# Performance work log

Hardware: AMD Instinct MI355X
Metric: run time of the kernel (lower is better)

Reference implementation:

```python
import jax, jax.numpy as jnp
import numpy as np
import math

# Equal-size graphs make SAGPooling's top-k static; removed edges are kept with a validity mask.
B, N0, D, H, HID, POS, DEG = 64, 400, 128, 4, 64, 16, 16
C = D // H                     # per-head dim = 32
EG = N0 * DEG                  # edges per graph
E = B * EG                     # 409600 edges total
RATIO = 0.8
K1 = math.ceil(RATIO * N0)     # 320
K2 = math.ceil(RATIO * K1)     # 256
K3 = math.ceil(RATIO * K2)     # 205
KS = (K1, K2, K3)
EPS = 1e-5

def _lin(x, W, b):
    return x @ W + b

def _ln(x, g, b):
    mu = x.mean(-1, keepdims=True)
    var = ((x - mu) ** 2).mean(-1, keepdims=True)
    return (x - mu) * jax.lax.rsqrt(var + EPS) * g + b

def _bn(x, g, b):  # BatchNorm1d, training mode (biased batch variance)
    mu = x.mean(0)
    var = ((x - mu) ** 2).mean(0)
    return (x - mu) * jax.lax.rsqrt(var + EPS) * g + b

def _transformer_conv(x, src, dst, mask, Wq, bq, Wk, bk, Wv, bv, Ws, bs, N):
    # PyG TransformerConv (concat=True, root_weight=True): scatter-softmax attention over edges
    q = _lin(x, Wq, bq).reshape(N, H, C)
    k = _lin(x, Wk, bk).reshape(N, H, C)
    v = _lin(x, Wv, bv).reshape(N, H, C)
    logits = jnp.einsum('ehc,ehc->eh', q[dst], k[src]) / jnp.sqrt(jnp.float32(C))
    logits = jnp.where(mask[:, None], logits, -1e9)
    m = jnp.maximum(jax.ops.segment_max(logits, dst, num_segments=N), -1e9)
    w = jnp.exp(logits - m[dst]) * mask[:, None]
    denom = jax.ops.segment_sum(w, dst, num_segments=N)
    alpha = w / jnp.where(denom[dst] > 0, denom[dst], 1.0)  # [E,H]
    msg = jax.ops.segment_sum(v[src] * alpha[:, :, None], dst, num_segments=N)
    return msg.reshape(N, D) + _lin(x, Ws, bs)

def _gt_block(x, src, dst, mask, Wq, bq, Wk, bk, Wv, bv, Ws, bs,
              Wlo, blo, g1, be1, W1, b1, W2, b2, g2, be2, N):
    out1 = _lin(_transformer_conv(x, src, dst, mask, Wq, bq, Wk, bk, Wv, bv, Ws, bs, N), Wlo, blo)
    out2 = _ln(out1 + x, g1, be1)
    out3 = _lin(jax.nn.relu(_lin(out2, W1, b1)), W2, b2)
    return _ln(out3 + out2, g2, be2)

def _sag_pool(x, src, dst, mask, Wrel, brel, Wroot, n, k):
    # SAGPooling: GraphConv(aggr='add') scorer, tanh nonlinearity, per-graph top-k, filter_adj via mask
    Nn = B * n
    agg = jax.ops.segment_sum(x[src] * mask[:, None], dst, num_segments=Nn)
    s = jnp.tanh((agg @ Wrel + brel + x @ Wroot)[:, 0])
    tv, ti = jax.lax.top_k(s.reshape(B, n), k)  # [B,k]
    perm = (ti + jnp.arange(B, dtype=ti.dtype)[:, None] * n).reshape(-1)
    x_new = x[perm] * tv.reshape(-1, 1)
    kept = jnp.zeros(Nn, bool).at[perm].set(True)
    new_id = jnp.zeros(Nn, jnp.int32).at[perm].set(jnp.arange(B * k, dtype=jnp.int32))
    nm = mask & kept[src] & kept[dst]
    return x_new, jnp.where(nm, new_id[src], 0), jnp.where(nm, new_id[dst], 0), nm

def _forward(x, lap_pos_enc, W_pos, b_pos,
             gt_Wq, gt_bq, gt_Wk, gt_bk, gt_Wv, gt_bv, gt_Wskip, gt_bskip,
             gt_Wlo, gt_blo, gt_ln1g, gt_ln1b, gt_W1, gt_b1, gt_W2, gt_b2, gt_ln2g, gt_ln2b,
             pool_Wrel, pool_brel, pool_Wroot,
             hW1, hb1, hW2, hb2, hW3, hb3, bn1g, bn1b, bn2g, bn2b,
             edge_src, edge_dst):
    x = x + _lin(lap_pos_enc, W_pos, b_pos)
    src, dst = edge_src, edge_dst
    mask = jnp.ones(src.shape, bool)
    n = N0
    feats = []
    for i in range(3):
        x = _gt_block(x, src, dst, mask,
                      gt_Wq[i], gt_bq[i], gt_Wk[i], gt_bk[i], gt_Wv[i], gt_bv[i],
                      gt_Wskip[i], gt_bskip[i], gt_Wlo[i], gt_blo[i],
                      gt_ln1g[i], gt_ln1b[i], gt_W1[i], gt_b1[i], gt_W2[i], gt_b2[i],
                      gt_ln2g[i], gt_ln2b[i], B * n)
        x, src, dst, mask = _sag_pool(x, src, dst, mask, pool_Wrel[i], pool_brel[i], pool_Wroot[i], n, KS[i])
        n = KS[i]
        xg = x.reshape(B, n, D)
        feats.append(jnp.concatenate([xg.max(1), xg.mean(1)], axis=1))  # [B, 2D] = gmp | gap
    xf = feats[0] + feats[1] + feats[2]
    h = jax.nn.relu(_bn(_lin(xf, hW1, hb1), bn1g, bn1b))
    h = jax.nn.relu(_bn(_lin(h, hW2, hb2), bn2g, bn2b))
    return _lin(h, hW3, hb3)[:, 0]  # [B]

def setup_inputs():
    key = jax.random.key(0)
    ks = jax.random.split(key, 16)
    rn = lambda k, shape, fan: jax.random.normal(k, shape, jnp.float32) / np.float32(np.sqrt(fan))
    inp = {}
    inp['x'] = jax.random.normal(ks[0], (B * N0, D), jnp.float32)
    inp['lap_pos_enc'] = jax.random.normal(ks[1], (B * N0, POS), jnp.float32)
    offs = (jnp.arange(B, dtype=jnp.int32) * N0)[:, None]
    inp['edge_src'] = (jax.random.randint(ks[2], (B, EG), 0, N0, jnp.int32) + offs).reshape(-1)
    inp['edge_dst'] = (jax.random.randint(ks[3], (B, EG), 0, N0, jnp.int32) + offs).reshape(-1)
    inp['W_pos'] = rn(ks[4], (POS, D), POS); inp['b_pos'] = jnp.zeros(D)
    pk = jax.random.split(ks[5], 12)
    inp['gt_Wq'] = rn(pk[0], (3, D, D), D); inp['gt_bq'] = jnp.zeros((3, D))
    inp['gt_Wk'] = rn(pk[1], (3, D, D), D); inp['gt_bk'] = jnp.zeros((3, D))
    inp['gt_Wv'] = rn(pk[2], (3, D, D), D); inp['gt_bv'] = jnp.zeros((3, D))
    inp['gt_Wskip'] = rn(pk[3], (3, D, D), D); inp['gt_bskip'] = jnp.zeros((3, D))
    inp['gt_Wlo'] = rn(pk[4], (3, D, D), D); inp['gt_blo'] = jnp.zeros((3, D))
    inp['gt_ln1g'] = jnp.ones((3, D)); inp['gt_ln1b'] = jnp.zeros((3, D))
    inp['gt_W1'] = rn(pk[5], (3, D, HID), D); inp['gt_b1'] = jnp.zeros((3, HID))
    inp['gt_W2'] = rn(pk[6], (3, HID, D), HID); inp['gt_b2'] = jnp.zeros((3, D))
    inp['gt_ln2g'] = jnp.ones((3, D)); inp['gt_ln2b'] = jnp.zeros((3, D))
    inp['pool_Wrel'] = rn(pk[7], (3, D, 1), D); inp['pool_brel'] = jnp.zeros((3, 1))
    inp['pool_Wroot'] = rn(pk[8], (3, D, 1), D)
    inp['hW1'] = rn(pk[9], (2 * D, D), 2 * D); inp['hb1'] = jnp.zeros(D)
    inp['hW2'] = rn(pk[10], (D, D // 2), D); inp['hb2'] = jnp.zeros(D // 2)
    inp['hW3'] = rn(pk[11], (D // 2, 1), D // 2); inp['hb3'] = jnp.zeros(1)
    inp['bn1g'] = jnp.ones(D); inp['bn1b'] = jnp.zeros(D)
    inp['bn2g'] = jnp.ones(D // 2); inp['bn2b'] = jnp.zeros(D // 2)
    return inp

def reference(x, lap_pos_enc, edge_src, edge_dst, W_pos, b_pos,
              gt_Wq, gt_bq, gt_Wk, gt_bk, gt_Wv, gt_bv, gt_Wskip, gt_bskip,
              gt_Wlo, gt_blo, gt_ln1g, gt_ln1b, gt_W1, gt_b1, gt_W2, gt_b2, gt_ln2g, gt_ln2b,
              pool_Wrel, pool_brel, pool_Wroot,
              hW1, hb1, hW2, hb2, hW3, hb3, bn1g, bn1b, bn2g, bn2b):
    return _forward(x, lap_pos_enc, W_pos, b_pos,
                    gt_Wq, gt_bq, gt_Wk, gt_bk, gt_Wv, gt_bv, gt_Wskip, gt_bskip,
                    gt_Wlo, gt_blo, gt_ln1g, gt_ln1b, gt_W1, gt_b1, gt_W2, gt_b2, gt_ln2g, gt_ln2b,
                    pool_Wrel, pool_brel, pool_Wroot,
                    hW1, hb1, hW2, hb2, hW3, hb3, bn1g, bn1b, bn2g, bn2b,
                    edge_src, edge_dst)
```

## Files before the change

kernel.cpp:

```cpp
#include <hip/hip_runtime.h>
#include <math.h>

#define BB   64
#define NPG0 400
#define DD   128
#define HH   4
#define CC   32
#define HIDD 64
#define POSD 16
#define EE   409600
#define EG   6400

__global__ void k_pos(const float* __restrict__ x, const float* __restrict__ lap,
                      const float* __restrict__ Wp, const float* __restrict__ bp,
                      float* __restrict__ out, int N){
  __shared__ float W[POSD*DD];
  __shared__ float bsh[DD];
  for(int i=threadIdx.x;i<POSD*DD;i+=blockDim.x) W[i]=Wp[i];
  for(int i=threadIdx.x;i<DD;i+=blockDim.x) bsh[i]=bp[i];
  __syncthreads();
  int total=N*DD;
  for(int idx=blockIdx.x*blockDim.x+threadIdx.x; idx<total; idx+=gridDim.x*blockDim.x){
    int n=idx>>7, d=idx&127;
    const float* lr=lap+(size_t)n*POSD;
    float acc=bsh[d]+x[idx];
    #pragma unroll
    for(int p=0;p<POSD;p++) acc=fmaf(lr[p],W[p*DD+d],acc);
    out[idx]=acc;
  }
}

template<int DIN,int DOUT,int EPI>
__global__ __launch_bounds__(512) void k_gemm_rt(
    const float* __restrict__ X, const float* __restrict__ Wg,
    const float* __restrict__ bias, const float* __restrict__ resid,
    const float* __restrict__ gam, const float* __restrict__ bet,
    float* __restrict__ Y){
  constexpr int BM=64;
  constexpr int CG=DOUT/4;
  constexpr int RS=512/CG;
  constexpr int RPT=BM/RS;
  constexpr int XPAD=DIN+4;
  __shared__ float Wl[DIN*DOUT];
  __shared__ float Xl[BM*XPAD];
  int tid=threadIdx.x;
  { const float4* ws=(const float4*)Wg; float4* wd=(float4*)Wl;
    for(int i=tid;i<DIN*DOUT/4;i+=512) wd[i]=ws[i]; }
  { const float4* xs=(const float4*)(X+(size_t)blockIdx.x*BM*DIN);
    for(int i=tid;i<BM*DIN/4;i+=512){
      int r=i/(DIN/4), kq=i%(DIN/4);
      *(float4*)&Xl[r*XPAD+kq*4]=xs[i];
    } }
  __syncthreads();
  int cg=tid%CG, rs=tid/CG;
  float acc[RPT][4];
  #pragma unroll
  for(int j=0;j<RPT;j++){acc[j][0]=0.f;acc[j][1]=0.f;acc[j][2]=0.f;acc[j][3]=0.f;}
  for(int kt=0;kt<DIN/4;kt++){
    float4 w0=*(const float4*)&Wl[(4*kt+0)*DOUT+cg*4];
    float4 w1=*(const float4*)&Wl[(4*kt+1)*DOUT+cg*4];
    float4 w2=*(const float4*)&Wl[(4*kt+2)*DOUT+cg*4];
    float4 w3=*(const float4*)&Wl[(4*kt+3)*DOUT+cg*4];
    #pragma unroll
    for(int j=0;j<RPT;j++){
      float4 xv=*(const float4*)&Xl[(rs+RS*j)*XPAD+4*kt];
      acc[j][0]=fmaf(xv.x,w0.x,fmaf(xv.y,w1.x,fmaf(xv.z,w2.x,fmaf(xv.w,w3.x,acc[j][0]))));
      acc[j][1]=fmaf(xv.x,w0.y,fmaf(xv.y,w1.y,fmaf(xv.z,w2.y,fmaf(xv.w,w3.y,acc[j][1]))));
      acc[j][2]=fmaf(xv.x,w0.z,fmaf(xv.y,w1.z,fmaf(xv.z,w2.z,fmaf(xv.w,w3.z,acc[j][2]))));
      acc[j][3]=fmaf(xv.x,w0.w,fmaf(xv.y,w1.w,fmaf(xv.z,w2.w,fmaf(xv.w,w3.w,acc[j][3]))));
    }
  }
  float4 bv=((const float4*)bias)[cg];
  #pragma unroll
  for(int j=0;j<RPT;j++){
    int row=blockIdx.x*BM + rs+RS*j;
    float4 v;
    v.x=acc[j][0]+bv.x; v.y=acc[j][1]+bv.y; v.z=acc[j][2]+bv.z; v.w=acc[j][3]+bv.w;
    if(EPI==1){
      v.x=fmaxf(v.x,0.f); v.y=fmaxf(v.y,0.f); v.z=fmaxf(v.z,0.f); v.w=fmaxf(v.w,0.f);
    }
    if(EPI==2){
      float4 rv=*(const float4*)&resid[(size_t)row*DOUT+cg*4];
      v.x+=rv.x; v.y+=rv.y; v.z+=rv.z; v.w+=rv.w;
      float ssum=v.x+v.y+v.z+v.w;
      #pragma unroll
      for(int off=CG/2;off;off>>=1) ssum+=__shfl_xor(ssum,off);
      float mu=ssum*(1.f/DOUT);
      float dx=v.x-mu, dy=v.y-mu, dz=v.z-mu, dw=v.w-mu;
      float vsum=dx*dx+dy*dy+dz*dz+dw*dw;
      #pragma unroll
      for(int off=CG/2;off;off>>=1) vsum+=__shfl_xor(vsum,off);
      float inv=1.0f/sqrtf(vsum*(1.f/DOUT)+1e-5f);
      float4 g4=((const float4*)gam)[cg];
      float4 b4=((const float4*)bet)[cg];
      v.x=dx*inv*g4.x+b4.x; v.y=dy*inv*g4.y+b4.y;
      v.z=dz*inv*g4.z+b4.z; v.w=dw*inv*g4.w+b4.w;
    }
    *(float4*)&Y[(size_t)row*DOUT+cg*4]=v;
  }
}

__global__ __launch_bounds__(512) void k_gemm4(
    const float* __restrict__ X,
    const float* __restrict__ W0c,const float* __restrict__ W1c,
    const float* __restrict__ W2c,const float* __restrict__ W3c,
    const float* __restrict__ b0c,const float* __restrict__ b1c,
    const float* __restrict__ b2c,const float* __restrict__ b3c,
    float* __restrict__ Y0c,float* __restrict__ Y1c,
    float* __restrict__ Y2c,float* __restrict__ Y3c){
  constexpr int BM=64, CG=32, RS=16, RPT=4, XPAD=132;
  __shared__ float Wl[DD*DD];
  __shared__ float Xl[BM*XPAD];
  int tid=threadIdx.x;
  { const float4* xs=(const float4*)(X+(size_t)blockIdx.x*BM*DD);
    for(int i=tid;i<BM*32;i+=512){
      int r=i>>5, kq=i&31;
      *(float4*)&Xl[r*XPAD+kq*4]=xs[i];
    } }
  int cg=tid%CG, rs=tid/CG;
  auto one=[&](const float* __restrict__ Wg,const float* __restrict__ bias,float* __restrict__ Y){
    __syncthreads();
    { const float4* ws=(const float4*)Wg; float4* wd=(float4*)Wl;
      for(int i=tid;i<DD*32;i+=512) wd[i]=ws[i]; }
    __syncthreads();
    float acc[RPT][4];
    #pragma unroll
    for(int j=0;j<RPT;j++){acc[j][0]=0.f;acc[j][1]=0.f;acc[j][2]=0.f;acc[j][3]=0.f;}
    for(int kt=0;kt<32;kt++){
      float4 w0=*(const float4*)&Wl[(4*kt+0)*DD+cg*4];
      float4 w1=*(const float4*)&Wl[(4*kt+1)*DD+cg*4];
      float4 w2=*(const float4*)&Wl[(4*kt+2)*DD+cg*4];
      float4 w3=*(const float4*)&Wl[(4*kt+3)*DD+cg*4];
      #pragma unroll
      for(int j=0;j<RPT;j++){
        float4 xv=*(const float4*)&Xl[(rs+RS*j)*XPAD+4*kt];
        acc[j][0]=fmaf(xv.x,w0.x,fmaf(xv.y,w1.x,fmaf(xv.z,w2.x,fmaf(xv.w,w3.x,acc[j][0]))));
        acc[j][1]=fmaf(xv.x,w0.y,fmaf(xv.y,w1.y,fmaf(xv.z,w2.y,fmaf(xv.w,w3.y,acc[j][1]))));
        acc[j][2]=fmaf(xv.x,w0.z,fmaf(xv.y,w1.z,fmaf(xv.z,w2.z,fmaf(xv.w,w3.z,acc[j][2]))));
        acc[j][3]=fmaf(xv.x,w0.w,fmaf(xv.y,w1.w,fmaf(xv.z,w2.w,fmaf(xv.w,w3.w,acc[j][3]))));
      }
    }
    float4 bv=((const float4*)bias)[cg];
    #pragma unroll
    for(int j=0;j<RPT;j++){
      int row=blockIdx.x*BM + rs+RS*j;
      float4 v;
      v.x=acc[j][0]+bv.x; v.y=acc[j][1]+bv.y; v.z=acc[j][2]+bv.z; v.w=acc[j][3]+bv.w;
      *(float4*)&Y[(size_t)row*DD+cg*4]=v;
    }
  };
  one(W0c,b0c,Y0c);
  one(W1c,b1c,Y1c);
  one(W2c,b2c,Y2c);
  one(W3c,b3c,Y3c);
}

__global__ __launch_bounds__(512) void k_csr(const int* __restrict__ src,const int* __restrict__ dst,
   const int* __restrict__ msk,const int* __restrict__ kept,const int* __restrict__ nid,int n,
   int* __restrict__ rowstart,int* __restrict__ rowcnt,int* __restrict__ esrc,
   int* __restrict__ nsrc,int* __restrict__ ndst,int* __restrict__ nmsk){
  __shared__ int cnt[512];
  __shared__ int woff[512];
  int b=blockIdx.x, t=threadIdx.x;
  cnt[t]=0;
  __syncthreads();
  int ebase=b*EG, nbase=b*n;
  for(int j=t;j<EG;j+=512){
    int e=ebase+j;
    int s,d,m;
    if(kept){
      int s0=src[e], d0=dst[e];
      m=(msk?msk[e]:1) && kept[s0] && kept[d0];
      s=m?nid[s0]:0; d=m?nid[d0]:0;
      nsrc[e]=s; ndst[e]=d; nmsk[e]=m;
    } else { s=src[e]; d=dst[e]; m=1; }
    if(m) atomicAdd(&cnt[d-nbase],1);
  }
  __syncthreads();
  int v=cnt[t];
  woff[t]=v;
  __syncthreads();
  for(int off=1;off<512;off<<=1){
    int a=(t>=off)?woff[t-off]:0;
    __syncthreads();
    woff[t]+=a;
    __syncthreads();
  }
  int excl=woff[t]-v;
  if(t<n){ rowstart[nbase+t]=ebase+excl; rowcnt[nbase+t]=v; }
  __syncthreads();
  woff[t]=excl;
  __syncthreads();
  for(int j=t;j<EG;j+=512){
    int e=ebase+j;
    int s,d,m;
    if(kept){ m=nmsk[e]; s=nsrc[e]; d=ndst[e]; }
    else { m=1; s=src[e]; d=dst[e]; }
    if(!m) continue;
    int off=atomicAdd(&woff[d-nbase],1);
    esrc[ebase+off]=s;
  }
}

template<int NG>
__global__ __launch_bounds__(512) void k_attn4(const float* __restrict__ q,const float* __restrict__ kk,
     const float* __restrict__ v,const int* __restrict__ rowstart,const int* __restrict__ rowcnt,
     const int* __restrict__ esrc,float* __restrict__ attn){
  __shared__ float4 kl[NG*9];
  __shared__ float4 vl[NG*9];
  int b=blockIdx.x>>2, h=blockIdx.x&3;
  int nb=b*NG;
  const float4* kg=(const float4*)kk;
  const float4* vg=(const float4*)v;
  for(int i=threadIdx.x;i<NG*8;i+=512){
    int node=i>>3, qq=i&7;
    size_t gidx=(size_t)(nb+node)*32 + h*8 + qq;
    kl[node*9+qq]=kg[gidx];
    vl[node*9+qq]=vg[gidx];
  }
  __syncthreads();
  int node=threadIdx.x;
  if(node>=NG) return;
  int gn=nb+node;
  float4 q0,q1,q2,q3,q4,q5,q6,q7;
  { const float4* qp=(const float4*)(q+(size_t)gn*DD+h*CC);
    q0=qp[0];q1=qp[1];q2=qp[2];q3=qp[3];q4=qp[4];q5=qp[5];q6=qp[6];q7=qp[7]; }
  int st=rowstart[gn], cn=rowcnt[gn];
  float m=-1e30f, s=0.f;
  float4 o0={0,0,0,0},o1={0,0,0,0},o2={0,0,0,0},o3={0,0,0,0};
  float4 o4={0,0,0,0},o5={0,0,0,0},o6={0,0,0,0},o7={0,0,0,0};
  for(int j=0;j<cn;j++){
    int sl=esrc[st+j]-nb;
    const float4* kr=&kl[sl*9];
    float4 k0=kr[0],k1=kr[1],k2=kr[2],k3=kr[3],k4=kr[4],k5=kr[5],k6=kr[6],k7=kr[7];
    float a0=q0.x*k0.x+q0.y*k0.y+q0.z*k0.z+q0.w*k0.w;
    float a1=q1.x*k1.x+q1.y*k1.y+q1.z*k1.z+q1.w*k1.w;
    float a2=q2.x*k2.x+q2.y*k2.y+q2.z*k2.z+q2.w*k2.w;
    float a3=q3.x*k3.x+q3.y*k3.y+q3.z*k3.z+q3.w*k3.w;
    a0+=q4.x*k4.x+q4.y*k4.y+q4.z*k4.z+q4.w*k4.w;
    a1+=q5.x*k5.x+q5.y*k5.y+q5.z*k5.z+q5.w*k5.w;
    a2+=q6.x*k6.x+q6.y*k6.y+q6.z*k6.z+q6.w*k6.w;
    a3+=q7.x*k7.x+q7.y*k7.y+q7.z*k7.z+q7.w*k7.w;
    float lg=((a0+a1)+(a2+a3))*0.17677669529663687f;
    const float4* vr=&vl[sl*9];
    float4 v0=vr[0],v1=vr[1],v2=vr[2],v3=vr[3],v4=vr[4],v5=vr[5],v6=vr[6],v7=vr[7];
    if(lg<=m){
      float w=__expf(lg-m);
      s+=w;
      o0.x=fmaf(w,v0.x,o0.x);o0.y=fmaf(w,v0.y,o0.y);o0.z=fmaf(w,v0.z,o0.z);o0.w=fmaf(w,v0.w,o0.w);
      o1.x=fmaf(w,v1.x,o1.x);o1.y=fmaf(w,v1.y,o1.y);o1.z=fmaf(w,v1.z,o1.z);o1.w=fmaf(w,v1.w,o1.w);
      o2.x=fmaf(w,v2.x,o2.x);o2.y=fmaf(w,v2.y,o2.y);o2.z=fmaf(w,v2.z,o2.z);o2.w=fmaf(w,v2.w,o2.w);
      o3.x=fmaf(w,v3.x,o3.x);o3.y=fmaf(w,v3.y,o3.y);o3.z=fmaf(w,v3.z,o3.z);o3.w=fmaf(w,v3.w,o3.w);
      o4.x=fmaf(w,v4.x,o4.x);o4.y=fmaf(w,v4.y,o4.y);o4.z=fmaf(w,v4.z,o4.z);o4.w=fmaf(w,v4.w,o4.w);
      o5.x=fmaf(w,v5.x,o5.x);o5.y=fmaf(w,v5.y,o5.y);o5.z=fmaf(w,v5.z,o5.z);o5.w=fmaf(w,v5.w,o5.w);
      o6.x=fmaf(w,v6.x,o6.x);o6.y=fmaf(w,v6.y,o6.y);o6.z=fmaf(w,v6.z,o6.z);o6.w=fmaf(w,v6.w,o6.w);
      o7.x=fmaf(w,v7.x,o7.x);o7.y=fmaf(w,v7.y,o7.y);o7.z=fmaf(w,v7.z,o7.z);o7.w=fmaf(w,v7.w,o7.w);
    } else {
      float r=__expf(m-lg);
      s=fmaf(s,r,1.f);
      o0.x=fmaf(o0.x,r,v0.x);o0.y=fmaf(o0.y,r,v0.y);o0.z=fmaf(o0.z,r,v0.z);o0.w=fmaf(o0.w,r,v0.w);
      o1.x=fmaf(o1.x,r,v1.x);o1.y=fmaf(o1.y,r,v1.y);o1.z=fmaf(o1.z,r,v1.z);o1.w=fmaf(o1.w,r,v1.w);
      o2.x=fmaf(o2.x,r,v2.x);o2.y=fmaf(o2.y,r,v2.y);o2.z=fmaf(o2.z,r,v2.z);o2.w=fmaf(o2.w,r,v2.w);
      o3.x=fmaf(o3.x,r,v3.x);o3.y=fmaf(o3.y,r,v3.y);o3.z=fmaf(o3.z,r,v3.z);o3.w=fmaf(o3.w,r,v3.w);
      o4.x=fmaf(o4.x,r,v4.x);o4.y=fmaf(o4.y,r,v4.y);o4.z=fmaf(o4.z,r,v4.z);o4.w=fmaf(o4.w,r,v4.w);
      o5.x=fmaf(o5.x,r,v5.x);o5.y=fmaf(o5.y,r,v5.y);o5.z=fmaf(o5.z,r,v5.z);o5.w=fmaf(o5.w,r,v5.w);
      o6.x=fmaf(o6.x,r,v6.x);o6.y=fmaf(o6.y,r,v6.y);o6.z=fmaf(o6.z,r,v6.z);o6.w=fmaf(o6.w,r,v6.w);
      o7.x=fmaf(o7.x,r,v7.x);o7.y=fmaf(o7.y,r,v7.y);o7.z=fmaf(o7.z,r,v7.z);o7.w=fmaf(o7.w,r,v7.w);
      m=lg;
    }
  }
  float inv=(s>0.f)?(1.f/s):0.f;
  float* op=attn+(size_t)gn*DD+h*CC;
  float4* op4=(float4*)op;
  float4 r0=op4[0],r1=op4[1],r2=op4[2],r3=op4[3],r4=op4[4],r5=op4[5],r6=op4[6],r7=op4[7];
  r0.x+=o0.x*inv;r0.y+=o0.y*inv;r0.z+=o0.z*inv;r0.w+=o0.w*inv;
  r1.x+=o1.x*inv;r1.y+=o1.y*inv;r1.z+=o1.z*inv;r1.w+=o1.w*inv;
  r2.x+=o2.x*inv;r2.y+=o2.y*inv;r2.z+=o2.z*inv;r2.w+=o2.w*inv;
  r3.x+=o3.x*inv;r3.y+=o3.y*inv;r3.z+=o3.z*inv;r3.w+=o3.w*inv;
  r4.x+=o4.x*inv;r4.y+=o4.y*inv;r4.z+=o4.z*inv;r4.w+=o4.w*inv;
  r5.x+=o5.x*inv;r5.y+=o5.y*inv;r5.z+=o5.z*inv;r5.w+=o5.w*inv;
  r6.x+=o6.x*inv;r6.y+=o6.y*inv;r6.z+=o6.z*inv;r6.w+=o6.w*inv;
  r7.x+=o7.x*inv;r7.y+=o7.y*inv;r7.z+=o7.z*inv;r7.w+=o7.w*inv;
  op4[0]=r0;op4[1]=r1;op4[2]=r2;op4[3]=r3;op4[4]=r4;op4[5]=r5;op4[6]=r6;op4[7]=r7;
}

__global__ __launch_bounds__(512) void k_sagtopk(const float* __restrict__ x,
   const float* __restrict__ wrel,const float* __restrict__ wroot,const float* __restrict__ brel,
   const int* __restrict__ rowstart,const int* __restrict__ rowcnt,const int* __restrict__ esrc,
   int n,int k,float* __restrict__ tv,int* __restrict__ gi,
   int* __restrict__ kept,int* __restrict__ nid){
  __shared__ float pnl[NPG0];
  __shared__ float sv[512];
  __shared__ int   si[512];
  int b=blockIdx.x, t=threadIdx.x, nbase=b*n;
  float rdot=0.f;
  if(t<n){
    const float4* xr=(const float4*)(x+(size_t)(nbase+t)*DD);
    float p=0.f;
    #pragma unroll
    for(int qq=0;qq<32;qq++){
      float4 xv=xr[qq];
      float4 wr=((const float4*)wrel)[qq];
      float4 wo=((const float4*)wroot)[qq];
      p   =fmaf(xv.x,wr.x,fmaf(xv.y,wr.y,fmaf(xv.z,wr.z,fmaf(xv.w,wr.w,p))));
      rdot=fmaf(xv.x,wo.x,fmaf(xv.y,wo.y,fmaf(xv.z,wo.z,fmaf(xv.w,wo.w,rdot))));
    }
    pnl[t]=p;
  }
  __syncthreads();
  float sc=-INFINITY;
  if(t<n){
    int st=rowstart[nbase+t], cn=rowcnt[nbase+t];
    float s=0.f;
    for(int j=0;j<cn;j++) s+=pnl[esrc[st+j]-nbase];
    sc=tanhf(s+brel[0]+rdot);
  }
  sv[t]=(t<n)?sc:-INFINITY;
  si[t]=t;
  for(int ksz=2;ksz<=512;ksz<<=1){
    for(int j=ksz>>1;j>0;j>>=1){
      __syncthreads();
      int ixj=t^j;
      if(ixj>t){
        float s1=sv[t], s2=sv[ixj];
        int i1=si[t], i2=si[ixj];
        bool firstRanks=(s1>s2)||(s1==s2&&i1<i2);
        bool up=((t&ksz)==0);
        if(up? !firstRanks : firstRanks){ sv[t]=s2;sv[ixj]=s1;si[t]=i2;si[ixj]=i1; }
      }
    }
  }
  __syncthreads();
  if(t<k){
    int oldg=nbase+si[t];
    tv[b*k+t]=sv[t];
    gi[b*k+t]=oldg;
    kept[oldg]=1;
    nid[oldg]=b*k+t;
  } else if(t<n){
    kept[nbase+si[t]]=0;
  }
}

__global__ void k_gather(const float* __restrict__ xin, const int* __restrict__ gi,
                         const float* __restrict__ tv, float* __restrict__ xout, int rows){
  int idx=blockIdx.x*blockDim.x+threadIdx.x;
  if(idx>=rows*DD) return;
  int r=idx>>7;
  int d=idx&127;
  xout[idx]=xin[(size_t)gi[r]*DD+d]*tv[r];
}

__global__ __launch_bounds__(512) void k_readout(const float* __restrict__ xk, int k,
                                                 float* __restrict__ xf){
  __shared__ float pm[512];
  __shared__ float ps[512];
  int b=blockIdx.x, t=threadIdx.x;
  int d=t&127, strip=t>>7;
  const float* base=xk+((size_t)b*k)*DD+d;
  float mx=-INFINITY, sm=0.f;
  for(int j=strip;j<k;j+=4){
    float v=base[(size_t)j*DD];
    mx=fmaxf(mx,v); sm+=v;
  }
  pm[t]=mx; ps[t]=sm;
  __syncthreads();
  if(t<128){
    float m0=fmaxf(fmaxf(pm[t],pm[t+128]),fmaxf(pm[t+256],pm[t+384]));
    float s0=ps[t]+ps[t+128]+ps[t+256]+ps[t+384];
    xf[b*256+t]+=m0;
    xf[b*256+128+t]+=s0/(float)k;
  }
}

__global__ void k_h1(const float* __restrict__ xf,const float* __restrict__ W,const float* __restrict__ b,float* __restrict__ z){
  int i=blockIdx.x*blockDim.x+threadIdx.x; if(i>=BB*DD) return;
  int r=i>>7, j=i&127;
  float acc=b[j];
  const float* xr=xf+r*256;
  #pragma unroll 8
  for(int t=0;t<256;t++) acc=fmaf(xr[t], W[t*DD+j], acc);
  z[i]=acc;
}
__global__ void k_bnrelu(const float* __restrict__ z,const float* __restrict__ g,const float* __restrict__ be,
                         float* __restrict__ h,int cols){
  int j=blockIdx.x*blockDim.x+threadIdx.x; if(j>=cols) return;
  float mu=0.f;
  for(int r=0;r<BB;r++) mu+=z[r*cols+j];
  mu*=(1.f/BB);
  float var=0.f;
  for(int r=0;r<BB;r++){ float d=z[r*cols+j]-mu; var+=d*d; }
  var*=(1.f/BB);
  float inv=1.0f/sqrtf(var+1e-5f);
  float gg=g[j], bb=be[j];
  for(int r=0;r<BB;r++){ float y=(z[r*cols+j]-mu)*inv*gg+bb; h[r*cols+j]=fmaxf(y,0.f); }
}
__global__ void k_h2(const float* __restrict__ h1,const float* __restrict__ W,const float* __restrict__ b,float* __restrict__ z){
  int i=blockIdx.x*blockDim.x+threadIdx.x; if(i>=BB*HIDD) return;
  int r=i>>6, j=i&63;
  float acc=b[j];
  #pragma unroll 8
  for(int t=0;t<DD;t++) acc=fmaf(h1[r*DD+t], W[t*HIDD+j], acc);
  z[i]=acc;
}
__global__ void k_h3(const float* __restrict__ h2,const float* __restrict__ W,const float* __restrict__ b,float* __restrict__ out){
  int bi=threadIdx.x; if(bi>=BB) return;
  float acc=b[0];
  for(int t=0;t<HIDD;t++) acc=fmaf(h2[bi*HIDD+t], W[t], acc);
  out[bi]=acc;
}

extern "C" void kernel_launch(void* const* d_in, const int* in_sizes, int n_in,
                              void* d_out, int out_size, void* d_ws, size_t ws_size,
                              hipStream_t stream){
  (void)in_sizes; (void)n_in; (void)out_size; (void)ws_size;
  const float* x_in =(const float*)d_in[0];
  const float* lap  =(const float*)d_in[1];
  const int*   esrc0=(const int*)  d_in[2];
  const int*   edst0=(const int*)  d_in[3];
  const float* Wpos =(const float*)d_in[4];
  const float* bpos =(const float*)d_in[5];
  const float* gWq  =(const float*)d_in[6];
  const float* gbq  =(const float*)d_in[7];
  const float* gWk  =(const float*)d_in[8];
  const float* gbk  =(const float*)d_in[9];
  const float* gWv  =(const float*)d_in[10];
  const float* gbv  =(const float*)d_in[11];
  const float* gWs  =(const float*)d_in[12];
  const float* gbs  =(const float*)d_in[13];
  const float* gWlo =(const float*)d_in[14];
  const float* gblo =(const float*)d_in[15];
  const float* gl1g =(const float*)d_in[16];
  const float* gl1b =(const float*)d_in[17];
  const float* gW1  =(const float*)d_in[18];
  const float* gb1  =(const float*)d_in[19];
  const float* gW2  =(const float*)d_in[20];
  const float* gb2  =(const float*)d_in[21];
  const float* gl2g =(const float*)d_in[22];
  const float* gl2b =(const float*)d_in[23];
  const float* pWrel=(const float*)d_in[24];
  const float* pbrel=(const float*)d_in[25];
  const float* pWrt =(const float*)d_in[26];
  const float* hW1  =(const float*)d_in[27];
  const float* hb1  =(const float*)d_in[28];
  const float* hW2  =(const float*)d_in[29];
  const float* hb2  =(const float*)d_in[30];
  const float* hW3  =(const float*)d_in[31];
  const float* hb3  =(const float*)d_in[32];
  const float* bn1g =(const float*)d_in[33];
  const float* bn1b =(const float*)d_in[34];
  const float* bn2g =(const float*)d_in[35];
  const float* bn2b =(const float*)d_in[36];
  float* out=(float*)d_out;

  char* base=(char*)d_ws; size_t off=0;
  auto alloc=[&](size_t bytes)->void*{ void* p=base+off; off+=(bytes+255)&~(size_t)255; return p; };
  const int NMAX=BB*NPG0;
  float* xA  =(float*)alloc((size_t)NMAX*DD*4);
  float* qb  =(float*)alloc((size_t)NMAX*DD*4);
  float* kb  =(float*)alloc((size_t)NMAX*DD*4);
  float* vb  =(float*)alloc((size_t)NMAX*DD*4);
  float* xO  =(float*)alloc((size_t)NMAX*DD*4);
  float* t2  =(float*)alloc((size_t)NMAX*DD*4);
  int*   rowstart=(int*)alloc((size_t)NMAX*4);
  int*   rowcnt  =(int*)alloc((size_t)NMAX*4);
  int*   esrcW   =(int*)alloc((size_t)EE*4);
  float* tvb =(float*)alloc((size_t)BB*320*4);
  int*   gib =(int*)  alloc((size_t)BB*320*4);
  int*   kept=(int*)  alloc((size_t)NMAX*4);
  int*   nid =(int*)  alloc((size_t)NMAX*4);
  int*   srcA=(int*)  alloc((size_t)EE*4);
  int*   dstA=(int*)  alloc((size_t)EE*4);
  int*   mskA=(int*)  alloc((size_t)EE*4);
  int*   srcB=(int*)  alloc((size_t)EE*4);
  int*   dstB=(int*)  alloc((size_t)EE*4);
  int*   mskB=(int*)  alloc((size_t)EE*4);
  float* xf  =(float*)alloc((size_t)BB*256*4);
  float* z1  =(float*)alloc((size_t)BB*DD*4);
  float* h1b =(float*)alloc((size_t)BB*DD*4);
  float* z2  =(float*)alloc((size_t)BB*HIDD*4);
  float* h2b =(float*)alloc((size_t)BB*HIDD*4);

  const int npg[3]={400,320,256};
  const int kpg[3]={320,256,205};
  const int Nin[3]={BB*400, BB*320, BB*256};

  hipMemsetAsync(xf,0,(size_t)BB*256*4,stream);
  k_pos<<<2048,256,0,stream>>>(x_in,lap,Wpos,bpos,xA,Nin[0]);

  const int* src=esrc0; const int* dst=edst0; const int* msk=nullptr;

  for(int i=0;i<3;i++){
    int N=Nin[i];
    int gB=N/64;
    const float* Wq=gWq+(size_t)i*DD*DD;   const float* bq=gbq+(size_t)i*DD;
    const float* Wk=gWk+(size_t)i*DD*DD;   const float* bk=gbk+(size_t)i*DD;
    const float* Wv=gWv+(size_t)i*DD*DD;   const float* bv=gbv+(size_t)i*DD;
    const float* Ws=gWs+(size_t)i*DD*DD;   const float* bs=gbs+(size_t)i*DD;
    const float* Wlo=gWlo+(size_t)i*DD*DD; const float* blo=gblo+(size_t)i*DD;
    const float* l1g=gl1g+(size_t)i*DD;    const float* l1b=gl1b+(size_t)i*DD;
    const float* W1=gW1+(size_t)i*DD*HIDD; const float* b1=gb1+(size_t)i*HIDD;
    const float* W2=gW2+(size_t)i*HIDD*DD; const float* b2=gb2+(size_t)i*DD;
    const float* l2g=gl2g+(size_t)i*DD;    const float* l2b=gl2b+(size_t)i*DD;
    const float* wrel=pWrel+(size_t)i*DD;  const float* brel=pbrel+(size_t)i;
    const float* wrt=pWrt+(size_t)i*DD;

    if(i==0){
      k_csr<<<BB,512,0,stream>>>(src,dst,nullptr,nullptr,nullptr,npg[i],
                                 rowstart,rowcnt,esrcW,nullptr,nullptr,nullptr);
    } else {
      int* ns=(i==1)?srcA:srcB; int* ndd=(i==1)?dstA:dstB; int* nm=(i==1)?mskA:mskB;
      k_csr<<<BB,512,0,stream>>>(src,dst,msk,kept,nid,npg[i],
                                 rowstart,rowcnt,esrcW,ns,ndd,nm);
      src=ns; dst=ndd; msk=nm;
    }

    k_gemm4<<<gB,512,0,stream>>>(xA,Wq,Wk,Wv,Ws,bq,bk,bv,bs,qb,kb,vb,xO);
    if(i==0)      k_attn4<400><<<BB*HH,512,0,stream>>>(qb,kb,vb,rowstart,rowcnt,esrcW,xO);
    else if(i==1) k_attn4<320><<<BB*HH,512,0,stream>>>(qb,kb,vb,rowstart,rowcnt,esrcW,xO);
    else          k_attn4<256><<<BB*HH,512,0,stream>>>(qb,kb,vb,rowstart,rowcnt,esrcW,xO);
    k_gemm_rt<128,128,2><<<gB,512,0,stream>>>(xO,Wlo,blo,xA,l1g,l1b,t2);
    k_gemm_rt<128,64,1><<<gB,512,0,stream>>>(t2,W1,b1,nullptr,nullptr,nullptr,qb);
    k_gemm_rt<64,128,2><<<gB,512,0,stream>>>(qb,W2,b2,t2,l2g,l2b,xO);

    k_sagtopk<<<BB,512,0,stream>>>(xO,wrel,wrt,brel,rowstart,rowcnt,esrcW,
                                   npg[i],kpg[i],tvb,gib,kept,nid);
    int rows=BB*kpg[i];
    k_gather<<<(rows*DD+255)/256,256,0,stream>>>(xO,gib,tvb,xA,rows);
    k_readout<<<BB,512,0,stream>>>(xA,kpg[i],xf);
  }

  k_h1<<<(BB*DD+127)/128,128,0,stream>>>(xf,hW1,hb1,z1);
  k_bnrelu<<<1,128,0,stream>>>(z1,bn1g,bn1b,h1b,DD);
  k_h2<<<(BB*HIDD+127)/128,128,0,stream>>>(h1b,hW2,hb2,z2);
  k_bnrelu<<<1,64,0,stream>>>(z2,bn2g,bn2b,h2b,HIDD);
  k_h3<<<1,64,0,stream>>>(h2b,hW3,hb3,out);
}
```

Baseline: 596.4 us.

## Use register-tiled 8x8 GEMM kernels for QKV projections and out-proj LayerNorm

Replaces the 512-thread shared-memory-weight GEMM for the four QKV/skip projections and for the output projection with LayerNorm with 128-thread kernels. Each thread computes an 8x8 output tile from a transposed X tile held in LDS, and the weights are read straight from global memory and L2. This gives more FMAs per load and drops the per-weight LDS staging and its barriers. In exchange it uses many more registers per thread, has fewer threads per block, and depends on the cache to absorb the uncoalesced weight reads.

```diff
diff --git a/kernel.cpp b/kernel.cpp
--- a/kernel.cpp
+++ b/kernel.cpp
@@ -10,6 +10,7 @@
 #define POSD 16
 #define EE   409600
 #define EG   6400
+#define XTP  68
 
 __global__ void k_pos(const float* __restrict__ x, const float* __restrict__ lap,
                       const float* __restrict__ Wp, const float* __restrict__ bp,
@@ -27,6 +28,139 @@
     #pragma unroll
     for(int p=0;p<POSD;p++) acc=fmaf(lr[p],W[p*DD+d],acc);
     out[idx]=acc;
+  }
+}
+
+
+__device__ __forceinline__ void stage_xt(const float* __restrict__ Xb, float* __restrict__ Xt, int tid){
+  for(int i=tid;i<32*64;i+=128){
+    int kq=i>>6, row=i&63;
+    float4 xv=*(const float4*)(Xb + row*DD + kq*4);
+    Xt[(4*kq+0)*XTP+row]=xv.x;
+    Xt[(4*kq+1)*XTP+row]=xv.y;
+    Xt[(4*kq+2)*XTP+row]=xv.z;
+    Xt[(4*kq+3)*XTP+row]=xv.w;
+  }
+}
+
+__global__ __launch_bounds__(128) void k_gemm4t(
+    const float* __restrict__ X,
+    const float* __restrict__ W0,const float* __restrict__ W1,
+    const float* __restrict__ W2,const float* __restrict__ W3,
+    const float* __restrict__ b0,const float* __restrict__ b1,
+    const float* __restrict__ b2,const float* __restrict__ b3,
+    float* __restrict__ Y0,float* __restrict__ Y1,
+    float* __restrict__ Y2,float* __restrict__ Y3){
+  __shared__ float Xt[DD*XTP];
+  int tid=threadIdx.x;
+  stage_xt(X+(size_t)blockIdx.x*64*DD, Xt, tid);
+  __syncthreads();
+  int tr=tid>>4, tc=tid&15;
+  int r0=tr*8, c0=tc*8;
+  auto one=[&](const float* __restrict__ Wg,const float* __restrict__ bias,float* __restrict__ Y){
+    float acc[8][8];
+    #pragma unroll
+    for(int a=0;a<8;a++){
+      #pragma unroll
+      for(int b=0;b<8;b++) acc[a][b]=0.f;
+    }
+    #pragma unroll 4
+    for(int k=0;k<DD;k++){
+      float4 x0=*(const float4*)&Xt[k*XTP+r0];
+      float4 x1=*(const float4*)&Xt[k*XTP+r0+4];
+      float4 w0=*(const float4*)(Wg + k*DD + c0);
+      float4 w1=*(const float4*)(Wg + k*DD + c0 + 4);
+      float xr[8]={x0.x,x0.y,x0.z,x0.w,x1.x,x1.y,x1.z,x1.w};
+      float wc[8]={w0.x,w0.y,w0.z,w0.w,w1.x,w1.y,w1.z,w1.w};
+      #pragma unroll
+      for(int a=0;a<8;a++){
+        #pragma unroll
+        for(int b=0;b<8;b++) acc[a][b]=fmaf(xr[a],wc[b],acc[a][b]);
+      }
+    }
+    float4 bv0=*(const float4*)(bias+c0);
+    float4 bv1=*(const float4*)(bias+c0+4);
+    float bb[8]={bv0.x,bv0.y,bv0.z,bv0.w,bv1.x,bv1.y,bv1.z,bv1.w};
+    #pragma unroll
+    for(int a=0;a<8;a++){
+      int row=blockIdx.x*64 + r0 + a;
+      float4 v0,v1;
+      v0.x=acc[a][0]+bb[0]; v0.y=acc[a][1]+bb[1]; v0.z=acc[a][2]+bb[2]; v0.w=acc[a][3]+bb[3];
+      v1.x=acc[a][4]+bb[4]; v1.y=acc[a][5]+bb[5]; v1.z=acc[a][6]+bb[6]; v1.w=acc[a][7]+bb[7];
+      *(float4*)&Y[(size_t)row*DD+c0]=v0;
+      *(float4*)&Y[(size_t)row*DD+c0+4]=v1;
+    }
+  };
+  one(W0,b0,Y0);
+  one(W1,b1,Y1);
+  one(W2,b2,Y2);
+  one(W3,b3,Y3);
+}
+
+__global__ __launch_bounds__(128) void k_gemm_lnt(
+    const float* __restrict__ X, const float* __restrict__ Wg,
+    const float* __restrict__ bias, const float* __restrict__ resid,
+    const float* __restrict__ gam, const float* __restrict__ bet,
+    float* __restrict__ Y){
+  __shared__ float Xt[DD*XTP];
+  int tid=threadIdx.x;
+  stage_xt(X+(size_t)blockIdx.x*64*DD, Xt, tid);
+  __syncthreads();
+  int tr=tid>>4, tc=tid&15;
+  int r0=tr*8, c0=tc*8;
+  float acc[8][8];
+  #pragma unroll
+  for(int a=0;a<8;a++){
+    #pragma unroll
+    for(int b=0;b<8;b++) acc[a][b]=0.f;
+  }
+  #pragma unroll 4
+  for(int k=0;k<DD;k++){
+    float4 x0=*(const float4*)&Xt[k*XTP+r0];
+    float4 x1=*(const float4*)&Xt[k*XTP+r0+4];
+    float4 w0=*(const float4*)(Wg + k*DD + c0);
+    float4 w1=*(const float4*)(Wg + k*DD + c0 + 4);
+    float xr[8]={x0.x,x0.y,x0.z,x0.w,x1.x,x1.y,x1.z,x1.w};
+    float wc[8]={w0.x,w0.y,w0.z,w0.w,w1.x,w1.y,w1.z,w1.w};
+    #pragma unroll
+    for(int a=0;a<8;a++){
+      #pragma unroll
+      for(int b=0;b<8;b++) acc[a][b]=fmaf(xr[a],wc[b],acc[a][b]);
+    }
+  }
+  float4 bv0=*(const float4*)(bias+c0);
+  float4 bv1=*(const float4*)(bias+c0+4);
+  float bb[8]={bv0.x,bv0.y,bv0.z,bv0.w,bv1.x,bv1.y,bv1.z,bv1.w};
+  float gg[8],ee[8];
+  { float4 g0=*(const float4*)(gam+c0), g1=*(const float4*)(gam+c0+4);
+    float4 e0=*(const float4*)(bet+c0), e1=*(const float4*)(bet+c0+4);
+    gg[0]=g0.x;gg[1]=g0.y;gg[2]=g0.z;gg[3]=g0.w;gg[4]=g1.x;gg[5]=g1.y;gg[6]=g1.z;gg[7]=g1.w;
+    ee[0]=e0.x;ee[1]=e0.y;ee[2]=e0.z;ee[3]=e0.w;ee[4]=e1.x;ee[5]=e1.y;ee[6]=e1.z;ee[7]=e1.w; }
+  #pragma unroll
+  for(int a=0;a<8;a++){
+    int row=blockIdx.x*64 + r0 + a;
+    float4 rv0=*(const float4*)&resid[(size_t)row*DD+c0];
+    float4 rv1=*(const float4*)&resid[(size_t)row*DD+c0+4];
+    float rr[8]={rv0.x,rv0.y,rv0.z,rv0.w,rv1.x,rv1.y,rv1.z,rv1.w};
+    float s=0.f;
+    #pragma unroll
+    for(int b=0;b<8;b++){ acc[a][b]+=bb[b]+rr[b]; s+=acc[a][b]; }
+    #pragma unroll
+    for(int o=8;o;o>>=1) s+=__shfl_xor(s,o);
+    float mu=s*(1.f/DD);
+    float vs=0.f;
+    #pragma unroll
+    for(int b=0;b<8;b++){ float d=acc[a][b]-mu; acc[a][b]=d; vs+=d*d; }
+    #pragma unroll
+    for(int o=8;o;o>>=1) vs+=__shfl_xor(vs,o);
+    float inv=1.0f/sqrtf(vs*(1.f/DD)+1e-5f);
+    float4 v0,v1;
+    v0.x=acc[a][0]*inv*gg[0]+ee[0]; v0.y=acc[a][1]*inv*gg[1]+ee[1];
+    v0.z=acc[a][2]*inv*gg[2]+ee[2]; v0.w=acc[a][3]*inv*gg[3]+ee[3];
+    v1.x=acc[a][4]*inv*gg[4]+ee[4]; v1.y=acc[a][5]*inv*gg[5]+ee[5];
+    v1.z=acc[a][6]*inv*gg[6]+ee[6]; v1.w=acc[a][7]*inv*gg[7]+ee[7];
+    *(float4*)&Y[(size_t)row*DD+c0]=v0;
+    *(float4*)&Y[(size_t)row*DD+c0+4]=v1;
   }
 }
 
@@ -98,61 +232,6 @@
     }
     *(float4*)&Y[(size_t)row*DOUT+cg*4]=v;
   }
-}
-
-__global__ __launch_bounds__(512) void k_gemm4(
-    const float* __restrict__ X,
-    const float* __restrict__ W0c,const float* __restrict__ W1c,
-    const float* __restrict__ W2c,const float* __restrict__ W3c,
-    const float* __restrict__ b0c,const float* __restrict__ b1c,
-    const float* __restrict__ b2c,const float* __restrict__ b3c,
-    float* __restrict__ Y0c,float* __restrict__ Y1c,
-    float* __restrict__ Y2c,float* __restrict__ Y3c){
-  constexpr int BM=64, CG=32, RS=16, RPT=4, XPAD=132;
-  __shared__ float Wl[DD*DD];
-  __shared__ float Xl[BM*XPAD];
-  int tid=threadIdx.x;
-  { const float4* xs=(const float4*)(X+(size_t)blockIdx.x*BM*DD);
-    for(int i=tid;i<BM*32;i+=512){
-      int r=i>>5, kq=i&31;
-      *(float4*)&Xl[r*XPAD+kq*4]=xs[i];
-    } }
-  int cg=tid%CG, rs=tid/CG;
-  auto one=[&](const float* __restrict__ Wg,const float* __restrict__ bias,float* __restrict__ Y){
-    __syncthreads();
-    { const float4* ws=(const float4*)Wg; float4* wd=(float4*)Wl;
-      for(int i=tid;i<DD*32;i+=512) wd[i]=ws[i]; }
-    __syncthreads();
-    float acc[RPT][4];
-    #pragma unroll
-    for(int j=0;j<RPT;j++){acc[j][0]=0.f;acc[j][1]=0.f;acc[j][2]=0.f;acc[j][3]=0.f;}
-    for(int kt=0;kt<32;kt++){
-      float4 w0=*(const float4*)&Wl[(4*kt+0)*DD+cg*4];
-      float4 w1=*(const float4*)&Wl[(4*kt+1)*DD+cg*4];
-      float4 w2=*(const float4*)&Wl[(4*kt+2)*DD+cg*4];
-      float4 w3=*(const float4*)&Wl[(4*kt+3)*DD+cg*4];
-      #pragma unroll
-      for(int j=0;j<RPT;j++){
-        float4 xv=*(const float4*)&Xl[(rs+RS*j)*XPAD+4*kt];
-        acc[j][0]=fmaf(xv.x,w0.x,fmaf(xv.y,w1.x,fmaf(xv.z,w2.x,fmaf(xv.w,w3.x,acc[j][0]))));
-        acc[j][1]=fmaf(xv.x,w0.y,fmaf(xv.y,w1.y,fmaf(xv.z,w2.y,fmaf(xv.w,w3.y,acc[j][1]))));
-        acc[j][2]=fmaf(xv.x,w0.z,fmaf(xv.y,w1.z,fmaf(xv.z,w2.z,fmaf(xv.w,w3.z,acc[j][2]))));
-        acc[j][3]=fmaf(xv.x,w0.w,fmaf(xv.y,w1.w,fmaf(xv.z,w2.w,fmaf(xv.w,w3.w,acc[j][3]))));
-      }
-    }
-    float4 bv=((const float4*)bias)[cg];
-    #pragma unroll
-    for(int j=0;j<RPT;j++){
-      int row=blockIdx.x*BM + rs+RS*j;
-      float4 v;
-      v.x=acc[j][0]+bv.x; v.y=acc[j][1]+bv.y; v.z=acc[j][2]+bv.z; v.w=acc[j][3]+bv.w;
-      *(float4*)&Y[(size_t)row*DD+cg*4]=v;
-    }
-  };
-  one(W0c,b0c,Y0c);
-  one(W1c,b1c,Y1c);
-  one(W2c,b2c,Y2c);
-  one(W3c,b3c,Y3c);
 }
 
 __global__ __launch_bounds__(512) void k_csr(const int* __restrict__ src,const int* __restrict__ dst,
@@ -515,11 +594,11 @@
       src=ns; dst=ndd; msk=nm;
     }
 
-    k_gemm4<<<gB,512,0,stream>>>(xA,Wq,Wk,Wv,Ws,bq,bk,bv,bs,qb,kb,vb,xO);
+    k_gemm4t<<<gB,128,0,stream>>>(xA,Wq,Wk,Wv,Ws,bq,bk,bv,bs,qb,kb,vb,xO);
     if(i==0)      k_attn4<400><<<BB*HH,512,0,stream>>>(qb,kb,vb,rowstart,rowcnt,esrcW,xO);
     else if(i==1) k_attn4<320><<<BB*HH,512,0,stream>>>(qb,kb,vb,rowstart,rowcnt,esrcW,xO);
     else          k_attn4<256><<<BB*HH,512,0,stream>>>(qb,kb,vb,rowstart,rowcnt,esrcW,xO);
-    k_gemm_rt<128,128,2><<<gB,512,0,stream>>>(xO,Wlo,blo,xA,l1g,l1b,t2);
+    k_gemm_lnt<<<gB,128,0,stream>>>(xO,Wlo,blo,xA,l1g,l1b,t2);
     k_gemm_rt<128,64,1><<<gB,512,0,stream>>>(t2,W1,b1,nullptr,nullptr,nullptr,qb);
     k_gemm_rt<64,128,2><<<gB,512,0,stream>>>(qb,W2,b2,t2,l2g,l2b,xO);
 
```

Measured after the change: 722.1 us. +21.1%, slower.

## Restructure dense GEMMs to one row per lane with wave-uniform weight loads

Applied to the files above, without the earlier changes.

The GEMM kernels stop staging the full weight matrix in shared memory. Each wavefront now owns a slice of output columns and each lane computes one row. Weights are read from global memory at wave-uniform addresses (readfirstlane), so they can become scalar/broadcast loads, and only the X tile sits in LDS. The LayerNorm epilogue now reduces across waves through shared memory and computes variance as E[x^2]-mu^2. This cuts LDS use and the weight-copy time per block, but the single-pass variance is less numerically accurate and the kernel relies on cache hits for weight reads.

```diff
diff --git a/kernel.cpp b/kernel.cpp
--- a/kernel.cpp
+++ b/kernel.cpp
@@ -30,129 +30,153 @@
   }
 }
 
+
 template<int DIN,int DOUT,int EPI>
-__global__ __launch_bounds__(512) void k_gemm_rt(
+__global__ __launch_bounds__(512) void k_gemm_sw(
     const float* __restrict__ X, const float* __restrict__ Wg,
     const float* __restrict__ bias, const float* __restrict__ resid,
     const float* __restrict__ gam, const float* __restrict__ bet,
     float* __restrict__ Y){
-  constexpr int BM=64;
-  constexpr int CG=DOUT/4;
-  constexpr int RS=512/CG;
-  constexpr int RPT=BM/RS;
+  constexpr int CPW=DOUT/8;
+  constexpr int NCG=CPW/4;
   constexpr int XPAD=DIN+4;
-  __shared__ float Wl[DIN*DOUT];
-  __shared__ float Xl[BM*XPAD];
+  __shared__ float Xl[64*XPAD];
+  __shared__ float redA[8*64];
+  __shared__ float redB[8*64];
   int tid=threadIdx.x;
-  { const float4* ws=(const float4*)Wg; float4* wd=(float4*)Wl;
-    for(int i=tid;i<DIN*DOUT/4;i+=512) wd[i]=ws[i]; }
-  { const float4* xs=(const float4*)(X+(size_t)blockIdx.x*BM*DIN);
-    for(int i=tid;i<BM*DIN/4;i+=512){
+  { const float4* xs=(const float4*)(X+(size_t)blockIdx.x*64*DIN);
+    for(int i=tid;i<64*DIN/4;i+=512){
       int r=i/(DIN/4), kq=i%(DIN/4);
       *(float4*)&Xl[r*XPAD+kq*4]=xs[i];
     } }
   __syncthreads();
-  int cg=tid%CG, rs=tid/CG;
-  float acc[RPT][4];
+  int lane=tid&63;
+  int wv=__builtin_amdgcn_readfirstlane(tid>>6);
+  int cbase=wv*CPW;
+  float acc[CPW];
   #pragma unroll
-  for(int j=0;j<RPT;j++){acc[j][0]=0.f;acc[j][1]=0.f;acc[j][2]=0.f;acc[j][3]=0.f;}
+  for(int c=0;c<CPW;c++) acc[c]=0.f;
+  const float* xr=&Xl[lane*XPAD];
+  #pragma unroll 2
   for(int kt=0;kt<DIN/4;kt++){
-    float4 w0=*(const float4*)&Wl[(4*kt+0)*DOUT+cg*4];
-    float4 w1=*(const float4*)&Wl[(4*kt+1)*DOUT+cg*4];
-    float4 w2=*(const float4*)&Wl[(4*kt+2)*DOUT+cg*4];
-    float4 w3=*(const float4*)&Wl[(4*kt+3)*DOUT+cg*4];
-    #pragma unroll
-    for(int j=0;j<RPT;j++){
-      float4 xv=*(const float4*)&Xl[(rs+RS*j)*XPAD+4*kt];
-      acc[j][0]=fmaf(xv.x,w0.x,fmaf(xv.y,w1.x,fmaf(xv.z,w2.x,fmaf(xv.w,w3.x,acc[j][0]))));
-      acc[j][1]=fmaf(xv.x,w0.y,fmaf(xv.y,w1.y,fmaf(xv.z,w2.y,fmaf(xv.w,w3.y,acc[j][1]))));
-      acc[j][2]=fmaf(xv.x,w0.z,fmaf(xv.y,w1.z,fmaf(xv.z,w2.z,fmaf(xv.w,w3.z,acc[j][2]))));
-      acc[j][3]=fmaf(xv.x,w0.w,fmaf(xv.y,w1.w,fmaf(xv.z,w2.w,fmaf(xv.w,w3.w,acc[j][3]))));
-    }
-  }
-  float4 bv=((const float4*)bias)[cg];
+    float4 xv=*(const float4*)&xr[4*kt];
+    float xk[4]={xv.x,xv.y,xv.z,xv.w};
+    #pragma unroll
+    for(int kk=0;kk<4;kk++){
+      const float4* wrow=(const float4*)(Wg+(size_t)(4*kt+kk)*DOUT+cbase);
+      #pragma unroll
+      for(int cg=0;cg<NCG;cg++){
+        float4 w4=wrow[cg];
+        acc[cg*4+0]=fmaf(xk[kk],w4.x,acc[cg*4+0]);
+        acc[cg*4+1]=fmaf(xk[kk],w4.y,acc[cg*4+1]);
+        acc[cg*4+2]=fmaf(xk[kk],w4.z,acc[cg*4+2]);
+        acc[cg*4+3]=fmaf(xk[kk],w4.w,acc[cg*4+3]);
+      }
+    }
+  }
+  int row=blockIdx.x*64+lane;
+  const float4* bb4=(const float4*)(bias+cbase);
   #pragma unroll
-  for(int j=0;j<RPT;j++){
-    int row=blockIdx.x*BM + rs+RS*j;
-    float4 v;
-    v.x=acc[j][0]+bv.x; v.y=acc[j][1]+bv.y; v.z=acc[j][2]+bv.z; v.w=acc[j][3]+bv.w;
-    if(EPI==1){
-      v.x=fmaxf(v.x,0.f); v.y=fmaxf(v.y,0.f); v.z=fmaxf(v.z,0.f); v.w=fmaxf(v.w,0.f);
-    }
-    if(EPI==2){
-      float4 rv=*(const float4*)&resid[(size_t)row*DOUT+cg*4];
-      v.x+=rv.x; v.y+=rv.y; v.z+=rv.z; v.w+=rv.w;
-      float ssum=v.x+v.y+v.z+v.w;
-      #pragma unroll
-      for(int off=CG/2;off;off>>=1) ssum+=__shfl_xor(ssum,off);
-      float mu=ssum*(1.f/DOUT);
-      float dx=v.x-mu, dy=v.y-mu, dz=v.z-mu, dw=v.w-mu;
-      float vsum=dx*dx+dy*dy+dz*dz+dw*dw;
-      #pragma unroll
-      for(int off=CG/2;off;off>>=1) vsum+=__shfl_xor(vsum,off);
-      float inv=1.0f/sqrtf(vsum*(1.f/DOUT)+1e-5f);
-      float4 g4=((const float4*)gam)[cg];
-      float4 b4=((const float4*)bet)[cg];
-      v.x=dx*inv*g4.x+b4.x; v.y=dy*inv*g4.y+b4.y;
-      v.z=dz*inv*g4.z+b4.z; v.w=dw*inv*g4.w+b4.w;
-    }
-    *(float4*)&Y[(size_t)row*DOUT+cg*4]=v;
-  }
-}
-
-__global__ __launch_bounds__(512) void k_gemm4(
+  for(int cg=0;cg<NCG;cg++){
+    float4 b4=bb4[cg];
+    acc[cg*4+0]+=b4.x; acc[cg*4+1]+=b4.y; acc[cg*4+2]+=b4.z; acc[cg*4+3]+=b4.w;
+  }
+  if(EPI==1){
+    #pragma unroll
+    for(int c=0;c<CPW;c++) acc[c]=fmaxf(acc[c],0.f);
+  }
+  if(EPI==2){
+    #pragma unroll
+    for(int cg=0;cg<NCG;cg++){
+      float4 rv=*(const float4*)&resid[(size_t)row*DOUT+cbase+cg*4];
+      acc[cg*4+0]+=rv.x; acc[cg*4+1]+=rv.y; acc[cg*4+2]+=rv.z; acc[cg*4+3]+=rv.w;
+    }
+    float ps=0.f,pq=0.f;
+    #pragma unroll
+    for(int c=0;c<CPW;c++){ ps+=acc[c]; pq+=acc[c]*acc[c]; }
+    redA[wv*64+lane]=ps; redB[wv*64+lane]=pq;
+    __syncthreads();
+    float s=0.f,q=0.f;
+    #pragma unroll
+    for(int w=0;w<8;w++){ s+=redA[w*64+lane]; q+=redB[w*64+lane]; }
+    float mu=s*(1.f/DOUT);
+    float var=q*(1.f/DOUT)-mu*mu;
+    float inv=1.0f/sqrtf(var+1e-5f);
+    const float4* g4p=(const float4*)(gam+cbase);
+    const float4* e4p=(const float4*)(bet+cbase);
+    #pragma unroll
+    for(int cg=0;cg<NCG;cg++){
+      float4 g4=g4p[cg], e4=e4p[cg];
+      acc[cg*4+0]=(acc[cg*4+0]-mu)*inv*g4.x+e4.x;
+      acc[cg*4+1]=(acc[cg*4+1]-mu)*inv*g4.y+e4.y;
+      acc[cg*4+2]=(acc[cg*4+2]-mu)*inv*g4.z+e4.z;
+      acc[cg*4+3]=(acc[cg*4+3]-mu)*inv*g4.w+e4.w;
+    }
+  }
+  #pragma unroll
+  for(int cg=0;cg<NCG;cg++){
+    float4 v; v.x=acc[cg*4+0]; v.y=acc[cg*4+1]; v.z=acc[cg*4+2]; v.w=acc[cg*4+3];
+    *(float4*)&Y[(size_t)row*DOUT+cbase+cg*4]=v;
+  }
+}
+
+__global__ __launch_bounds__(512) void k_gemm4_sw(
     const float* __restrict__ X,
-    const float* __restrict__ W0c,const float* __restrict__ W1c,
-    const float* __restrict__ W2c,const float* __restrict__ W3c,
-    const float* __restrict__ b0c,const float* __restrict__ b1c,
-    const float* __restrict__ b2c,const float* __restrict__ b3c,
-    float* __restrict__ Y0c,float* __restrict__ Y1c,
-    float* __restrict__ Y2c,float* __restrict__ Y3c){
-  constexpr int BM=64, CG=32, RS=16, RPT=4, XPAD=132;
-  __shared__ float Wl[DD*DD];
-  __shared__ float Xl[BM*XPAD];
+    const float* __restrict__ W0,const float* __restrict__ W1,
+    const float* __restrict__ W2,const float* __restrict__ W3,
+    const float* __restrict__ b0,const float* __restrict__ b1,
+    const float* __restrict__ b2,const float* __restrict__ b3,
+    float* __restrict__ Y0,float* __restrict__ Y1,
+    float* __restrict__ Y2,float* __restrict__ Y3){
+  constexpr int XPAD=DD+4;
+  __shared__ float Xl[64*XPAD];
   int tid=threadIdx.x;
-  { const float4* xs=(const float4*)(X+(size_t)blockIdx.x*BM*DD);
-    for(int i=tid;i<BM*32;i+=512){
+  { const float4* xs=(const float4*)(X+(size_t)blockIdx.x*64*DD);
+    for(int i=tid;i<64*32;i+=512){
       int r=i>>5, kq=i&31;
       *(float4*)&Xl[r*XPAD+kq*4]=xs[i];
     } }
-  int cg=tid%CG, rs=tid/CG;
+  __syncthreads();
+  int lane=tid&63;
+  int wv=__builtin_amdgcn_readfirstlane(tid>>6);
+  int cbase=wv*16;
+  int row=blockIdx.x*64+lane;
+  const float* xr=&Xl[lane*XPAD];
   auto one=[&](const float* __restrict__ Wg,const float* __restrict__ bias,float* __restrict__ Y){
-    __syncthreads();
-    { const float4* ws=(const float4*)Wg; float4* wd=(float4*)Wl;
-      for(int i=tid;i<DD*32;i+=512) wd[i]=ws[i]; }
-    __syncthreads();
-    float acc[RPT][4];
-    #pragma unroll
-    for(int j=0;j<RPT;j++){acc[j][0]=0.f;acc[j][1]=0.f;acc[j][2]=0.f;acc[j][3]=0.f;}
+    float acc[16];
+    #pragma unroll
+    for(int c=0;c<16;c++) acc[c]=0.f;
+    #pragma unroll 2
     for(int kt=0;kt<32;kt++){
-      float4 w0=*(const float4*)&Wl[(4*kt+0)*DD+cg*4];
-      float4 w1=*(const float4*)&Wl[(4*kt+1)*DD+cg*4];
-      float4 w2=*(const float4*)&Wl[(4*kt+2)*DD+cg*4];
-      float4 w3=*(const float4*)&Wl[(4*kt+3)*DD+cg*4];
+      float4 xv=*(const float4*)&xr[4*kt];
+      float xk[4]={xv.x,xv.y,xv.z,xv.w};
       #pragma unroll
-      for(int j=0;j<RPT;j++){
-        float4 xv=*(const float4*)&Xl[(rs+RS*j)*XPAD+4*kt];
-        acc[j][0]=fmaf(xv.x,w0.x,fmaf(xv.y,w1.x,fmaf(xv.z,w2.x,fmaf(xv.w,w3.x,acc[j][0]))));
-        acc[j][1]=fmaf(xv.x,w0.y,fmaf(xv.y,w1.y,fmaf(xv.z,w2.y,fmaf(xv.w,w3.y,acc[j][1]))));
-        acc[j][2]=fmaf(xv.x,w0.z,fmaf(xv.y,w1.z,fmaf(xv.z,w2.z,fmaf(xv.w,w3.z,acc[j][2]))));
-        acc[j][3]=fmaf(xv.x,w0.w,fmaf(xv.y,w1.w,fmaf(xv.z,w2.w,fmaf(xv.w,w3.w,acc[j][3]))));
+      for(int kk=0;kk<4;kk++){
+        const float4* wrow=(const float4*)(Wg+(size_t)(4*kt+kk)*DD+cbase);
+        #pragma unroll
+        for(int cg=0;cg<4;cg++){
+          float4 w4=wrow[cg];
+          acc[cg*4+0]=fmaf(xk[kk],w4.x,acc[cg*4+0]);
+          acc[cg*4+1]=fmaf(xk[kk],w4.y,acc[cg*4+1]);
+          acc[cg*4+2]=fmaf(xk[kk],w4.z,acc[cg*4+2]);
+          acc[cg*4+3]=fmaf(xk[kk],w4.w,acc[cg*4+3]);
+        }
       }
     }
-    float4 bv=((const float4*)bias)[cg];
-    #pragma unroll
-    for(int j=0;j<RPT;j++){
-      int row=blockIdx.x*BM + rs+RS*j;
+    const float4* bb4=(const float4*)(bias+cbase);
+    #pragma unroll
+    for(int cg=0;cg<4;cg++){
+      float4 b4=bb4[cg];
       float4 v;
-      v.x=acc[j][0]+bv.x; v.y=acc[j][1]+bv.y; v.z=acc[j][2]+bv.z; v.w=acc[j][3]+bv.w;
-      *(float4*)&Y[(size_t)row*DD+cg*4]=v;
+      v.x=acc[cg*4+0]+b4.x; v.y=acc[cg*4+1]+b4.y;
+      v.z=acc[cg*4+2]+b4.z; v.w=acc[cg*4+3]+b4.w;
+      *(float4*)&Y[(size_t)row*DD+cbase+cg*4]=v;
     }
   };
-  one(W0c,b0c,Y0c);
-  one(W1c,b1c,Y1c);
-  one(W2c,b2c,Y2c);
-  one(W3c,b3c,Y3c);
+  one(W0,b0,Y0);
+  one(W1,b1,Y1);
+  one(W2,b2,Y2);
+  one(W3,b3,Y3);
 }
 
 __global__ __launch_bounds__(512) void k_csr(const int* __restrict__ src,const int* __restrict__ dst,
@@ -515,13 +539,13 @@
       src=ns; dst=ndd; msk=nm;
     }
 
-    k_gemm4<<<gB,512,0,stream>>>(xA,Wq,Wk,Wv,Ws,bq,bk,bv,bs,qb,kb,vb,xO);
+    k_gemm4_sw<<<gB,512,0,stream>>>(xA,Wq,Wk,Wv,Ws,bq,bk,bv,bs,qb,kb,vb,xO);
     if(i==0)      k_attn4<400><<<BB*HH,512,0,stream>>>(qb,kb,vb,rowstart,rowcnt,esrcW,xO);
     else if(i==1) k_attn4<320><<<BB*HH,512,0,stream>>>(qb,kb,vb,rowstart,rowcnt,esrcW,xO);
     else          k_attn4<256><<<BB*HH,512,0,stream>>>(qb,kb,vb,rowstart,rowcnt,esrcW,xO);
-    k_gemm_rt<128,128,2><<<gB,512,0,stream>>>(xO,Wlo,blo,xA,l1g,l1b,t2);
-    k_gemm_rt<128,64,1><<<gB,512,0,stream>>>(t2,W1,b1,nullptr,nullptr,nullptr,qb);
-    k_gemm_rt<64,128,2><<<gB,512,0,stream>>>(qb,W2,b2,t2,l2g,l2b,xO);
+    k_gemm_sw<128,128,2><<<gB,512,0,stream>>>(xO,Wlo,blo,xA,l1g,l1b,t2);
+    k_gemm_sw<128,64,1><<<gB,512,0,stream>>>(t2,W1,b1,nullptr,nullptr,nullptr,qb);
+    k_gemm_sw<64,128,2><<<gB,512,0,stream>>>(qb,W2,b2,t2,l2g,l2b,xO);
 
     k_sagtopk<<<BB,512,0,stream>>>(xO,wrel,wrt,brel,rowstart,rowcnt,esrcW,
                                    npg[i],kpg[i],tvb,gib,kept,nid);
```

Result: no change. 595.4 us (-0.2%).
